# Performance work log

Hardware: AMD Instinct MI355X
Metric: run time of the kernel (lower is better)

Reference implementation:

```python
import jax, jax.numpy as jnp
import numpy as np

N_USER = 100_000
N_WALLET = 100_000
E = 1_600_000
HID, OUT = 128, 64
H, C = 4, 32  # GAT heads, per-head channels (HID // 4)
U_IN, W_IN = 16, 4
EPS = 1e-5


def _sage(x_src, x_dst, ei, w_l, b_l, w_r):
    """PyG SAGEConv (mean aggr): lin_l(mean_j x_j) + lin_r(x_i)."""
    src, dst = ei[0], ei[1]
    n = x_dst.shape[0]
    s = jax.ops.segment_sum(x_src[src], dst, num_segments=n)
    deg = jax.ops.segment_sum(jnp.ones((src.shape[0],), x_src.dtype), dst, num_segments=n)
    agg = s / jnp.maximum(deg, 1.0)[:, None]
    return agg @ w_l + b_l + x_dst @ w_r


def _bn(x, g, b):
    """BatchNorm over node dim (training-mode batch stats)."""
    m = x.mean(0)
    v = x.var(0)
    return (x - m) * jax.lax.rsqrt(v + EPS) * g + b


def _segment_softmax(logits, seg, n):
    m = jax.ops.segment_max(logits, seg, num_segments=n)
    e = jnp.exp(logits - m[seg])
    s = jax.ops.segment_sum(e, seg, num_segments=n)
    return e / (s[seg] + 1e-16)


def _gat(x, ei, w, a_src, a_dst, bias):
    """PyG GATConv with self-loops, heads concatenated. Dropout off (eval)."""
    n = x.shape[0]
    loop = jnp.arange(n, dtype=ei.dtype)
    src = jnp.concatenate([ei[0], loop])
    dst = jnp.concatenate([ei[1], loop])
    xp = (x @ w).reshape(n, H, C)                      # [n,H,C]
    al_s = (xp * a_src).sum(-1)                        # [n,H]
    al_d = (xp * a_dst).sum(-1)                        # [n,H]
    logits = jax.nn.leaky_relu(al_s[src] + al_d[dst], 0.2)  # [E+n,H]
    alpha = _segment_softmax(logits, dst, n)
    out = jax.ops.segment_sum(xp[src] * alpha[:, :, None], dst, num_segments=n)
    return out.reshape(n, H * C) + bias


def setup_inputs() -> dict:
    key = jax.random.key(0)
    ks = jax.random.split(key, 24)
    rn = lambda k, s, sc=0.05: jax.random.normal(k, s, jnp.float32) * sc
    ei = lambda k, n: jax.random.randint(k, (2, E), 0, n, jnp.int32)
    return {
        "x_user": rn(ks[0], (N_USER, U_IN), 1.0),
        "x_wallet": rn(ks[1], (N_WALLET, W_IN), 1.0),
        "w_u2w_l": rn(ks[2], (U_IN, HID)), "b_u2w": jnp.zeros((HID,), jnp.float32), "w_u2w_r": rn(ks[3], (W_IN, HID)),
        "w_w2u_l": rn(ks[4], (W_IN, HID)), "b_w2u": jnp.zeros((HID,), jnp.float32), "w_w2u_r": rn(ks[5], (U_IN, HID)),
        "w_u2u_l": rn(ks[6], (U_IN, HID)), "b_u2u": jnp.zeros((HID,), jnp.float32), "w_u2u_r": rn(ks[7], (U_IN, HID)),
        "bn_u_g": jnp.ones((HID,), jnp.float32), "bn_u_b": jnp.zeros((HID,), jnp.float32),
        "bn_w_g": jnp.ones((HID,), jnp.float32), "bn_w_b": jnp.zeros((HID,), jnp.float32),
        "gat_w": rn(ks[8], (HID, H * C)), "gat_as": rn(ks[9], (H, C)), "gat_ad": rn(ks[10], (H, C)),
        "gat_b": jnp.zeros((HID,), jnp.float32),
        "bn2_g": jnp.ones((HID,), jnp.float32), "bn2_b": jnp.zeros((HID,), jnp.float32),
        "proj_w": rn(ks[11], (HID, OUT)), "proj_b": jnp.zeros((OUT,), jnp.float32),
        "ei_uw": ei(ks[12], N_USER),   # src user -> dst wallet (both 100k)
        "ei_wu": ei(ks[13], N_WALLET),  # src wallet -> dst user
        "ei_uu": ei(ks[14], N_USER),
    }


def reference(x_user, x_wallet, w_u2w_l, b_u2w, w_u2w_r, w_w2u_l, b_w2u, w_w2u_r,
              w_u2u_l, b_u2u, w_u2u_r, bn_u_g, bn_u_b, bn_w_g, bn_w_b,
              gat_w, gat_as, gat_ad, gat_b, bn2_g, bn2_b, proj_w, proj_b,
              ei_uw, ei_wu, ei_uu):
    h_w_from_u = jax.nn.relu(_sage(x_user, x_wallet, ei_uw, w_u2w_l, b_u2w, w_u2w_r))
    h_u_from_w = jax.nn.relu(_sage(x_wallet, x_user, ei_wu, w_w2u_l, b_w2u, w_w2u_r))
    h_u_from_u = jax.nn.relu(_sage(x_user, x_user, ei_uu, w_u2u_l, b_u2u, w_u2u_r))
    h_user = _bn(h_u_from_w + h_u_from_u, bn_u_g, bn_u_b)
    _ = _bn(h_w_from_u, bn_w_g, bn_w_b)  # h_wallet: computed in torch module but unused in output
    h_user = jax.nn.relu(_gat(h_user, ei_uu, gat_w, gat_as, gat_ad, gat_b))
    h_user = _bn(h_user, bn2_g, bn2_b)
    return jax.nn.relu(h_user @ proj_w + proj_b)  # dropout = identity (eval)
```

## Files before the change

kernel.cpp:

```cpp
#include <hip/hip_runtime.h>
#include <hip/hip_bf16.h>
#include <cstdint>
#include <cstddef>

#define NN   100000
#define NE   1600000
#define CAP  48

#define NBKT 784
#define BSH  7
#define FB   8
#define BCAP 2432
#define ACHUNK 2048
#define NABLK 784

#define NTILES 1563
#define CH_BN 50
#define NSHAD 4
#define LOG2E 1.44269504088896f

typedef __attribute__((ext_vector_type(8))) short short8;
typedef __attribute__((ext_vector_type(4))) float floatx4;

__device__ inline short f2bs(float x) {
    __hip_bfloat16 h = __float2bfloat16(x);
    return *reinterpret_cast<short*>(&h);
}
__device__ inline int pack2(float a, float b) {
    return ((int)(unsigned short)f2bs(b) << 16) | (unsigned short)f2bs(a);
}
__device__ inline float bflo(unsigned p) { return __uint_as_float(p << 16); }
__device__ inline float bfhi(unsigned p) { return __uint_as_float(p & 0xFFFF0000u); }

#define OFF_PRE   ((size_t)0)
#define OFF_BKTU  ((size_t)0)
#define OFF_BKTW  ((size_t)1906688)
#define OFF_XP    ((size_t)12800000)
#define OFF_AGGU  ((size_t)12800000)
#define OFF_AGGW  ((size_t)14400000)
#define OFF_COLU  ((size_t)19200000)
#define OFF_S1    ((size_t)24000000)
#define OFF_Q1    ((size_t)24000512)
#define OFF_S2    ((size_t)24001024)
#define OFF_Q2    ((size_t)24001536)
#define OFF_CNTU  ((size_t)25600000)
#define OFF_BCUR  ((size_t)25800000)
#define OFF_ALS   ((size_t)25802112)
#define OFF_ALD   ((size_t)26202112)
#define ZBASE     OFF_BCUR
#define ZFLOATS   ((size_t)1600)
#define ZSTATS    ((size_t)2048)

__global__ void __launch_bounds__(256) bin_edges(
    const int* __restrict__ ei_u, const int* __restrict__ ei_w,
    int* __restrict__ bcur_u, int* __restrict__ bkt_u,
    int* __restrict__ bcur_w, int* __restrict__ bkt_w) {
    const int* ei = blockIdx.y ? ei_w : ei_u;
    int* bcur = blockIdx.y ? bcur_w : bcur_u;
    int* bkt  = blockIdx.y ? bkt_w  : bkt_u;
    __shared__ int lcnt[NBKT];
    __shared__ int lbuf[NBKT * FB];
    for (int i = threadIdx.x; i < NBKT; i += 256) lcnt[i] = 0;
    __syncthreads();
    int base = blockIdx.x * ACHUNK;
    #pragma unroll
    for (int k = 0; k < ACHUNK / 256; k++) {
        int e = base + k * 256 + threadIdx.x;
        if (e < NE) {
            int src = ei[e], dst = ei[NE + e];
            int b = dst >> BSH;
            int pk = ((dst & ((1 << BSH) - 1)) << 17) | src;
            int pos = atomicAdd(&lcnt[b], 1);
            if (pos < FB) lbuf[b * FB + pos] = pk;
            else {
                int g = atomicAdd(&bcur[b], 1);
                if (g < BCAP) bkt[(size_t)b * BCAP + g] = pk;
            }
        }
    }
    __syncthreads();
    int wid = threadIdx.x >> 6, lane = threadIdx.x & 63;
    const int BPW = NBKT / 4;
    int b0w = wid * BPW;
    for (int r = 0; r < BPW; r += 64) {
        int rb = r + lane;
        if (rb < BPW) {
            int b = b0w + rb;
            int c = lcnt[b];
            int nn2 = c < FB ? c : FB;
            if (nn2 > 0) {
                int g0 = atomicAdd(&bcur[b], nn2);
                for (int i2 = 0; i2 < nn2; i2++) {
                    int g = g0 + i2;
                    if (g < BCAP) bkt[(size_t)b * BCAP + g] = lbuf[b * FB + i2];
                }
            }
        }
    }
}

__global__ void __launch_bounds__(256) csr_agg(
    const int* __restrict__ bcur_u, const int* __restrict__ bkt_u,
    int* __restrict__ cnt_g, int* __restrict__ col_g,
    const float* __restrict__ xu, float* __restrict__ aggu,
    const int* __restrict__ bcur_w, const int* __restrict__ bkt_w,
    const float* __restrict__ xw, float* __restrict__ aggw) {
    int type = blockIdx.y;
    const int* bcur = type ? bcur_w : bcur_u;
    const int* bkt  = type ? bkt_w  : bkt_u;
    int B = blockIdx.x;
    int node_base = B << BSH;
    if (node_base >= NN) return;
    __shared__ int cnt[128];
    __shared__ int col[128 * CAP];
    if (threadIdx.x < 128) cnt[threadIdx.x] = 0;
    __syncthreads();
    int n = bcur[B]; if (n > BCAP) n = BCAP;
    const int* bp = bkt + (size_t)B * BCAP;
    for (int i = threadIdx.x; i < n; i += 256) {
        int p = bp[i];
        int d = p >> 17;
        int pos = atomicAdd(&cnt[d], 1);
        if (pos < CAP) col[d * CAP + pos] = p & 0x1FFFF;
    }
    __syncthreads();
    int nn_here = NN - node_base; if (nn_here > 128) nn_here = 128;
    int wv = threadIdx.x >> 6, lane = threadIdx.x & 63;

    if (type == 0) {
        if (threadIdx.x < nn_here) cnt_g[node_base + threadIdx.x] = cnt[threadIdx.x];
        int total4 = nn_here * CAP / 4;
        const int4* cs = (const int4*)col;
        int4* cg = (int4*)(col_g + (size_t)node_base * CAP);
        for (int i = threadIdx.x; i < total4; i += 256) cg[i] = cs[i];
        int j = lane >> 4, k = lane & 15;
        for (int nl = wv * 32; nl < wv * 32 + 32 && nl < nn_here; nl++) {
            int deg = cnt[nl];
            int nu = deg < CAP ? deg : CAP;
            float v0 = 0.f, v1 = 0.f, v2 = 0.f, v3 = 0.f;
            int iters = (nu + 15) >> 4;
            for (int it = 0; it < iters; it++) {
                int bb = j + (it << 4);
                int s0 = (bb < nu)      ? col[nl * CAP + bb]      : 0;
                int s1 = (bb + 4 < nu)  ? col[nl * CAP + bb + 4]  : 0;
                int s2 = (bb + 8 < nu)  ? col[nl * CAP + bb + 8]  : 0;
                int s3 = (bb + 12 < nu) ? col[nl * CAP + bb + 12] : 0;
                float x0 = xu[(size_t)s0 * 16 + k];
                float x1 = xu[(size_t)s1 * 16 + k];
                float x2 = xu[(size_t)s2 * 16 + k];
                float x3 = xu[(size_t)s3 * 16 + k];
                if (bb < nu)      v0 += x0;
                if (bb + 4 < nu)  v1 += x1;
                if (bb + 8 < nu)  v2 += x2;
                if (bb + 12 < nu) v3 += x3;
            }
            float v = (v0 + v1) + (v2 + v3);
            v += __shfl_xor(v, 16, 64);
            v += __shfl_xor(v, 32, 64);
            if (lane < 16)
                aggu[(size_t)(node_base + nl) * 16 + lane] = v / fmaxf((float)deg, 1.f);
        }
    } else {
        int j = lane >> 2, k = lane & 3;
        for (int nl = wv * 32; nl < wv * 32 + 32 && nl < nn_here; nl++) {
            int deg = cnt[nl];
            int nw = deg < CAP ? deg : CAP;
            float v = 0.f;
            int iters = (nw + 15) >> 4;
            for (int it = 0; it < iters; it++) {
                int bb = j + (it << 4);
                int s = (bb < nw) ? col[nl * CAP + bb] : 0;
                float x = xw[(size_t)s * 4 + k];
                if (bb < nw) v += x;
            }
            v += __shfl_xor(v, 4, 64);
            v += __shfl_xor(v, 8, 64);
            v += __shfl_xor(v, 16, 64);
            v += __shfl_xor(v, 32, 64);
            if (lane < 4)
                aggw[(size_t)(node_base + nl) * 4 + lane] = v / fmaxf((float)deg, 1.f);
        }
    }
}

__global__ void __launch_bounds__(256, 2) sage_gemm(
    const float* __restrict__ aggu, const float* __restrict__ aggw,
    const float* __restrict__ xu,
    const float* __restrict__ wl_w2u, const float* __restrict__ b_w2u, const float* __restrict__ wr_w2u,
    const float* __restrict__ wl_u2u, const float* __restrict__ b_u2u, const float* __restrict__ wr_u2u,
    __hip_bfloat16* __restrict__ pre) {
    __shared__ short lw[16 * 64 * 8];
    __shared__ short la[64 * 136];
    int tid = threadIdx.x;
    for (int idx = tid; idx < 8192; idx += 256) {
        int mat = idx >> 12;
        int k = (idx >> 7) & 31, n = idx & 127;
        float w;
        if (mat == 0)
            w = (k < 4) ? wl_w2u[k * 128 + n] : (k < 20 ? wr_w2u[(k - 4) * 128 + n] : 0.f);
        else
            w = (k < 16) ? wl_u2u[k * 128 + n] : wr_u2u[(k - 16) * 128 + n];
        int t = n >> 4, l15 = n & 15, q = (k >> 3) & 3, j = k & 7;
        lw[((mat * 8 + t) * 64 + q * 16 + l15) * 8 + j] = f2bs(w);
    }
    __syncthreads();
    int wv = tid >> 6, lane = tid & 63;
    int quad = lane >> 4, l15 = lane & 15;
    short8 w1[8], w2[8];
    #pragma unroll
    for (int t = 0; t < 8; t++) {
        w1[t] = *(const short8*)&lw[(t * 64 + lane) * 8];
        w2[t] = *(const short8*)&lw[((8 + t) * 64 + lane) * 8];
    }
    float bw[8], bu[8];
    #pragma unroll
    for (int t = 0; t < 8; t++) {
        bw[t] = b_w2u[t * 16 + l15];
        bu[t] = b_u2u[t * 16 + l15];
    }
    for (int tile = blockIdx.x; tile < NTILES; tile += gridDim.x) {
        int nbase = tile * 64;
        __syncthreads();
        {
            int node = tid >> 2, p = tid & 3;
            int gn = nbase + node;
            float4 v = make_float4(0.f, 0.f, 0.f, 0.f);
            if (gn < NN) v = *(const float4*)&xu[(size_t)gn * 16 + 4 * p];
            int2 pk; pk.x = pack2(v.x, v.y); pk.y = pack2(v.z, v.w);
            *(int2*)&la[node * 136 + 4 + 4 * p] = pk;
            *(int2*)&la[node * 136 + 48 + 4 * p] = pk;
        }
        {
            int node = tid >> 2, p = tid & 3;
            int gn = nbase + node;
            float4 v = make_float4(0.f, 0.f, 0.f, 0.f);
            if (gn < NN) v = *(const float4*)&aggu[(size_t)gn * 16 + 4 * p];
            int2 pk; pk.x = pack2(v.x, v.y); pk.y = pack2(v.z, v.w);
            *(int2*)&la[node * 136 + 32 + 4 * p] = pk;
        }
        if (tid < 64) {
            int node = tid, gn = nbase + node;
            float4 v = make_float4(0.f, 0.f, 0.f, 0.f);
            if (gn < NN) v = *(const float4*)&aggw[(size_t)gn * 4];
            int2 pk; pk.x = pack2(v.x, v.y); pk.y = pack2(v.z, v.w);
            *(int2*)&la[node * 136 + 0] = pk;
            int2 z; z.x = 0; z.y = 0;
            *(int2*)&la[node * 136 + 20] = z;
            *(int2*)&la[node * 136 + 24] = z;
            *(int2*)&la[node * 136 + 28] = z;
        }
        __syncthreads();
        short8 af1 = *(const short8*)&la[(wv * 16 + l15) * 136 + quad * 8];
        short8 af2 = *(const short8*)&la[(wv * 16 + l15) * 136 + 32 + quad * 8];
        floatx4 acc1[8], acc2[8];
        #pragma unroll
        for (int t = 0; t < 8; t++) {
            acc1[t] = (floatx4){0.f, 0.f, 0.f, 0.f};
            acc2[t] = (floatx4){0.f, 0.f, 0.f, 0.f};
        }
        #pragma unroll
        for (int t = 0; t < 8; t++) {
            acc1[t] = __builtin_amdgcn_mfma_f32_16x16x32_bf16(af1, w1[t], acc1[t], 0, 0, 0);
            acc2[t] = __builtin_amdgcn_mfma_f32_16x16x32_bf16(af2, w2[t], acc2[t], 0, 0, 0);
        }
        __syncthreads();
        #pragma unroll
        for (int t = 0; t < 8; t++)
            #pragma unroll
            for (int r = 0; r < 4; r++) {
                float v1 = fmaxf(acc1[t][r] + bw[t], 0.f);
                float v2 = fmaxf(acc2[t][r] + bu[t], 0.f);
                la[(wv * 16 + quad * 4 + r) * 136 + t * 16 + l15] = f2bs(v1 + v2);
            }
        __syncthreads();
        #pragma unroll
        for (int c = 0; c < 4; c++) {
            int idx = c * 256 + tid;
            int node = idx >> 4, f8 = (idx & 15) * 8;
            int gn = nbase + node;
            if (gn < NN)
                *(int4*)(pre + (size_t)gn * 128 + f8) = *(const int4*)&la[node * 136 + f8];
        }
    }
}

__global__ void __launch_bounds__(256) bn_stats_pre2(const unsigned* __restrict__ x2,
                                                     float* __restrict__ sum, float* __restrict__ sq) {
    int f2 = threadIdx.x & 63, half = threadIdx.x >> 6;
    int n0 = blockIdx.x * CH_BN;
    float s0 = 0.f, q0 = 0.f, s1 = 0.f, q1 = 0.f;
    for (int i = n0 + half; i < n0 + CH_BN; i += 4) {
        unsigned p = x2[(size_t)i * 64 + f2];
        float v0 = bflo(p), v1 = bfhi(p);
        s0 += v0; q0 += v0 * v0; s1 += v1; q1 += v1 * v1;
    }
    __shared__ float a0[256], c0[256], a1[256], c1[256];
    a0[threadIdx.x] = s0; c0[threadIdx.x] = q0;
    a1[threadIdx.x] = s1; c1[threadIdx.x] = q1;
    __syncthreads();
    if (half == 0) {
        for (int h = 1; h < 4; h++) {
            s0 += a0[h * 64 + f2]; q0 += c0[h * 64 + f2];
            s1 += a1[h * 64 + f2]; q1 += c1[h * 64 + f2];
        }
        int sh = (blockIdx.x & (NSHAD - 1)) << 7;
        atomicAdd(&sum[sh + 2 * f2], s0);     atomicAdd(&sq[sh + 2 * f2], q0);
        atomicAdd(&sum[sh + 2 * f2 + 1], s1); atomicAdd(&sq[sh + 2 * f2 + 1], q1);
    }
}

__global__ void __launch_bounds__(256) bn_stats_act2(const unsigned* __restrict__ x2,
                                                     const float* __restrict__ gb,
                                                     float* __restrict__ sum, float* __restrict__ sq) {
    int f2 = threadIdx.x & 63, half = threadIdx.x >> 6;
    int n0 = blockIdx.x * CH_BN;
    float gb0 = gb[2 * f2], gb1 = gb[2 * f2 + 1];
    float s0 = 0.f, q0 = 0.f, s1 = 0.f, q1 = 0.f;
    for (int i = n0 + half; i < n0 + CH_BN; i += 4) {
        unsigned p = x2[(size_t)i * 64 + f2];
        float v0 = fmaxf(bflo(p) + gb0, 0.f), v1 = fmaxf(bfhi(p) + gb1, 0.f);
        s0 += v0; q0 += v0 * v0; s1 += v1; q1 += v1 * v1;
    }
    __shared__ float a0[256], c0[256], a1[256], c1[256];
    a0[threadIdx.x] = s0; c0[threadIdx.x] = q0;
    a1[threadIdx.x] = s1; c1[threadIdx.x] = q1;
    __syncthreads();
    if (half == 0) {
        for (int h = 1; h < 4; h++) {
            s0 += a0[h * 64 + f2]; q0 += c0[h * 64 + f2];
            s1 += a1[h * 64 + f2]; q1 += c1[h * 64 + f2];
        }
        int sh = (blockIdx.x & (NSHAD - 1)) << 7;
        atomicAdd(&sum[sh + 2 * f2], s0);     atomicAdd(&sq[sh + 2 * f2], q0);
        atomicAdd(&sum[sh + 2 * f2 + 1], s1); atomicAdd(&sq[sh + 2 * f2 + 1], q1);
    }
}

__global__ void __launch_bounds__(256, 2) gemm_al(
    const unsigned* __restrict__ pre2, const float* __restrict__ s1, const float* __restrict__ q1,
    const float* __restrict__ bng, const float* __restrict__ bnb,
    const float* __restrict__ gw, const float* __restrict__ gas, const float* __restrict__ gad,
    __hip_bfloat16* __restrict__ xp, float* __restrict__ al_s, float* __restrict__ al_d) {
    __shared__ short lw[32 * 64 * 8];
    __shared__ short la[64 * 136];
    __shared__ float lsc[128], lsh[128];
    int tid = threadIdx.x;
    if (tid < 128) {
        float sv = s1[tid] + s1[128 + tid] + s1[256 + tid] + s1[384 + tid];
        float qv = q1[tid] + q1[128 + tid] + q1[256 + tid] + q1[384 + tid];
        float m = sv * (1.0f / NN);
        float v = qv * (1.0f / NN) - m * m;
        float sc = bng[tid] * rsqrtf(v + 1e-5f);
        lsc[tid] = sc; lsh[tid] = bnb[tid] - m * sc;
    }
    for (int idx = tid; idx < 16384; idx += 256) {
        int k = idx >> 7, n = idx & 127;
        int t = n >> 4, l15 = n & 15, s = k >> 5, q = (k >> 3) & 3, j = k & 7;
        lw[(((t * 4 + s) * 64) + q * 16 + l15) * 8 + j] = f2bs(gw[idx]);
    }
    __syncthreads();
    int wv = tid >> 6, lane = tid & 63;
    int quad = lane >> 4, l15 = lane & 15;
    short8 wfrag[8][4];
    #pragma unroll
    for (int t = 0; t < 8; t++)
        #pragma unroll
        for (int s = 0; s < 4; s++)
            wfrag[t][s] = *(const short8*)&lw[((t * 4 + s) * 64 + lane) * 8];
    float asv[8], adv[8];
    #pragma unroll
    for (int t = 0; t < 8; t++) {
        asv[t] = gas[t * 16 + l15] * LOG2E;
        adv[t] = gad[t * 16 + l15] * LOG2E;
    }
    for (int tile = blockIdx.x; tile < NTILES; tile += gridDim.x) {
        int nbase = tile * 64;
        __syncthreads();
        #pragma unroll
        for (int c = 0; c < 8; c++) {
            int idx = c * 256 + tid;
            int node = idx >> 5, g = idx & 31;
            uint2 pp = make_uint2(0u, 0u);
            int gn = nbase + node;
            if (gn < NN) pp = *(const uint2*)&pre2[(size_t)gn * 64 + 2 * g];
            int f = 4 * g;
            float v0 = bflo(pp.x), v1 = bfhi(pp.x), v2 = bflo(pp.y), v3 = bfhi(pp.y);
            int2 pk;
            pk.x = pack2(v0 * lsc[f] + lsh[f],         v1 * lsc[f + 1] + lsh[f + 1]);
            pk.y = pack2(v2 * lsc[f + 2] + lsh[f + 2], v3 * lsc[f + 3] + lsh[f + 3]);
            *(int2*)&la[node * 136 + f] = pk;
        }
        __syncthreads();
        short8 af[4];
        #pragma unroll
        for (int s = 0; s < 4; s++)
            af[s] = *(const short8*)&la[(wv * 16 + l15) * 136 + s * 32 + quad * 8];
        floatx4 acc[8];
        #pragma unroll
        for (int t = 0; t < 8; t++) acc[t] = (floatx4){0.f, 0.f, 0.f, 0.f};
        #pragma unroll
        for (int s = 0; s < 4; s++)
            #pragma unroll
            for (int t = 0; t < 8; t++)
                acc[t] = __builtin_amdgcn_mfma_f32_16x16x32_bf16(af[s], wfrag[t][s], acc[t], 0, 0, 0);
        #pragma unroll
        for (int r = 0; r < 4; r++) {
            int node = nbase + wv * 16 + quad * 4 + r;
            #pragma unroll
            for (int h = 0; h < 4; h++) {
                float vs = acc[2 * h][r] * asv[2 * h] + acc[2 * h + 1][r] * asv[2 * h + 1];
                float vd = acc[2 * h][r] * adv[2 * h] + acc[2 * h + 1][r] * adv[2 * h + 1];
                #pragma unroll
                for (int m = 8; m >= 1; m >>= 1) {
                    vs += __shfl_xor(vs, m, 64);
                    vd += __shfl_xor(vd, m, 64);
                }
                if (l15 == 0 && node < NN) {
                    al_s[(size_t)node * 4 + h] = vs;
                    al_d[(size_t)node * 4 + h] = vd;
                }
            }
        }
        __syncthreads();
        #pragma unroll
        for (int t = 0; t < 8; t++)
            #pragma unroll
            for (int r = 0; r < 4; r++)
                la[(wv * 16 + quad * 4 + r) * 136 + t * 16 + l15] = f2bs(acc[t][r]);
        __syncthreads();
        #pragma unroll
        for (int c = 0; c < 4; c++) {
            int idx = c * 256 + tid;
            int node = idx >> 4, f8 = (idx & 15) * 8;
            int gn = nbase + node;
            if (gn < NN)
                *(int4*)(xp + (size_t)gn * 128 + f8) = *(const int4*)&la[node * 136 + f8];
        }
    }
}

__global__ void __launch_bounds__(256, 2) gemm_proj(
    const unsigned* __restrict__ gat2, const float* __restrict__ gb,
    const float* __restrict__ s2, const float* __restrict__ q2,
    const float* __restrict__ bng, const float* __restrict__ bnb,
    const float* __restrict__ pw, const float* __restrict__ pb,
    float* __restrict__ out) {
    __shared__ short lw[16 * 64 * 8];
    __shared__ short la[64 * 136];
    __shared__ float lsc[128], lsh[128], lgb[128];
    int tid = threadIdx.x;
    if (tid < 128) {
        float sv = s2[tid] + s2[128 + tid] + s2[256 + tid] + s2[384 + tid];
        float qv = q2[tid] + q2[128 + tid] + q2[256 + tid] + q2[384 + tid];
        float m = sv * (1.0f / NN);
        float v = qv * (1.0f / NN) - m * m;
        float sc = bng[tid] * rsqrtf(v + 1e-5f);
        lsc[tid] = sc; lsh[tid] = bnb[tid] - m * sc;
        lgb[tid] = gb[tid];
    }
    for (int idx = tid; idx < 8192; idx += 256) {
        int k = idx >> 6, n = idx & 63;
        int t = n >> 4, l15 = n & 15, s = k >> 5, q = (k >> 3) & 3, j = k & 7;
        lw[(((t * 4 + s) * 64) + q * 16 + l15) * 8 + j] = f2bs(pw[idx]);
    }
    __syncthreads();
    int wv = tid >> 6, lane = tid & 63;
    int quad = lane >> 4, l15 = lane & 15;
    short8 wfrag[4][4];
    #pragma unroll
    for (int t = 0; t < 4; t++)
        #pragma unroll
        for (int s = 0; s < 4; s++)
            wfrag[t][s] = *(const short8*)&lw[((t * 4 + s) * 64 + lane) * 8];
    float pbv[4];
    #pragma unroll
    for (int t = 0; t < 4; t++) pbv[t] = pb[t * 16 + l15];
    for (int tile = blockIdx.x; tile < NTILES; tile += gridDim.x) {
        int nbase = tile * 64;
        __syncthreads();
        #pragma unroll
        for (int c = 0; c < 8; c++) {
            int idx = c * 256 + tid;
            int node = idx >> 5, g = idx & 31;
            uint2 pp = make_uint2(0u, 0u);
            int gn = nbase + node;
            if (gn < NN) pp = *(const uint2*)&gat2[(size_t)gn * 64 + 2 * g];
            int f = 4 * g;
            float h0 = fmaxf(bflo(pp.x) + lgb[f],     0.f) * lsc[f]     + lsh[f];
            float h1 = fmaxf(bfhi(pp.x) + lgb[f + 1], 0.f) * lsc[f + 1] + lsh[f + 1];
            float h2 = fmaxf(bflo(pp.y) + lgb[f + 2], 0.f) * lsc[f + 2] + lsh[f + 2];
            float h3 = fmaxf(bfhi(pp.y) + lgb[f + 3], 0.f) * lsc[f + 3] + lsh[f + 3];
            int2 pk; pk.x = pack2(h0, h1); pk.y = pack2(h2, h3);
            *(int2*)&la[node * 136 + f] = pk;
        }
        __syncthreads();
        short8 af[4];
        #pragma unroll
        for (int s = 0; s < 4; s++)
            af[s] = *(const short8*)&la[(wv * 16 + l15) * 136 + s * 32 + quad * 8];
        floatx4 acc[4];
        #pragma unroll
        for (int t = 0; t < 4; t++) acc[t] = (floatx4){0.f, 0.f, 0.f, 0.f};
        #pragma unroll
        for (int s = 0; s < 4; s++)
            #pragma unroll
            for (int t = 0; t < 4; t++)
                acc[t] = __builtin_amdgcn_mfma_f32_16x16x32_bf16(af[s], wfrag[t][s], acc[t], 0, 0, 0);
        #pragma unroll
        for (int r = 0; r < 4; r++) {
            int gn = nbase + wv * 16 + quad * 4 + r;
            if (gn < NN) {
                #pragma unroll
                for (int t = 0; t < 4; t++)
                    out[(size_t)gn * 64 + t * 16 + l15] = fmaxf(acc[t][r] + pbv[t], 0.f);
            }
        }
    }
}

__global__ void __launch_bounds__(256) gat_gather(
    const int* __restrict__ cnt_u, const int* __restrict__ col_u,
    const float* __restrict__ al_s, const float* __restrict__ al_d,
    const unsigned* __restrict__ xp2, unsigned* __restrict__ gout2) {
    int i = (blockIdx.x * 256 + threadIdx.x) >> 6;
    int lane = threadIdx.x & 63;
    int g = lane >> 4, q = lane & 15;
    int h = q >> 2;
    float ad = al_d[(size_t)i * 4 + h];
    int deg = cnt_u[i];
    int n = deg < CAP ? deg : CAP;
    int mycol = (lane < n) ? col_u[(size_t)i * CAP + lane] : 0;
    float a0 = 0.f, a1 = 0.f, a2 = 0.f, a3 = 0.f;
    float a4 = 0.f, a5 = 0.f, a6 = 0.f, a7 = 0.f, den = 0.f;
    if (g == 0) {
        float l = al_s[(size_t)i * 4 + h] + ad;
        float e = exp2f(fmaxf(l, 0.2f * l));
        uint4 p = *(const uint4*)&xp2[(size_t)i * 64 + 4 * q];
        a0 = e * bflo(p.x); a1 = e * bfhi(p.x);
        a2 = e * bflo(p.y); a3 = e * bfhi(p.y);
        a4 = e * bflo(p.z); a5 = e * bfhi(p.z);
        a6 = e * bflo(p.w); a7 = e * bfhi(p.w);
        den = e;
    }
    for (int b = 0; b < n; b += 16) {
        int s[4]; float A[4]; uint4 p[4];
        #pragma unroll
        for (int u = 0; u < 4; u++)
            s[u] = __shfl(mycol, b + 4 * u + g, 64);
        #pragma unroll
        for (int u = 0; u < 4; u++)
            A[u] = al_s[(size_t)s[u] * 4 + h];
        #pragma unroll
        for (int u = 0; u < 4; u++)
            p[u] = *(const uint4*)&xp2[(size_t)s[u] * 64 + 4 * q];
        #pragma unroll
        for (int u = 0; u < 4; u++) {
            float l = A[u] + ad;
            float e = (b + 4 * u + g < n) ? exp2f(fmaxf(l, 0.2f * l)) : 0.f;
            a0 += e * bflo(p[u].x); a1 += e * bfhi(p[u].x);
            a2 += e * bflo(p[u].y); a3 += e * bfhi(p[u].y);
            a4 += e * bflo(p[u].z); a5 += e * bfhi(p[u].z);
            a6 += e * bflo(p[u].w); a7 += e * bfhi(p[u].w);
            den += e;
        }
    }
    a0 += __shfl_xor(a0, 16, 64); a0 += __shfl_xor(a0, 32, 64);
    a1 += __shfl_xor(a1, 16, 64); a1 += __shfl_xor(a1, 32, 64);
    a2 += __shfl_xor(a2, 16, 64); a2 += __shfl_xor(a2, 32, 64);
    a3 += __shfl_xor(a3, 16, 64); a3 += __shfl_xor(a3, 32, 64);
    a4 += __shfl_xor(a4, 16, 64); a4 += __shfl_xor(a4, 32, 64);
    a5 += __shfl_xor(a5, 16, 64); a5 += __shfl_xor(a5, 32, 64);
    a6 += __shfl_xor(a6, 16, 64); a6 += __shfl_xor(a6, 32, 64);
    a7 += __shfl_xor(a7, 16, 64); a7 += __shfl_xor(a7, 32, 64);
    den += __shfl_xor(den, 16, 64); den += __shfl_xor(den, 32, 64);
    if (g == 0) {
        float r = 1.0f / (den + 1e-16f);
        uint4 o;
        o.x = (unsigned)pack2(a0 * r, a1 * r);
        o.y = (unsigned)pack2(a2 * r, a3 * r);
        o.z = (unsigned)pack2(a4 * r, a5 * r);
        o.w = (unsigned)pack2(a6 * r, a7 * r);
        *(uint4*)&gout2[(size_t)i * 64 + 4 * q] = o;
    }
}

extern "C" void kernel_launch(void* const* d_in, const int* in_sizes, int n_in,
                              void* d_out, int out_size, void* d_ws, size_t ws_size,
                              hipStream_t stream) {
    const float* x_user   = (const float*)d_in[0];
    const float* x_wallet = (const float*)d_in[1];
    const float* w_w2u_l  = (const float*)d_in[5];
    const float* b_w2u    = (const float*)d_in[6];
    const float* w_w2u_r  = (const float*)d_in[7];
    const float* w_u2u_l  = (const float*)d_in[8];
    const float* b_u2u    = (const float*)d_in[9];
    const float* w_u2u_r  = (const float*)d_in[10];
    const float* bn_u_g   = (const float*)d_in[11];
    const float* bn_u_b   = (const float*)d_in[12];
    const float* gat_w    = (const float*)d_in[15];
    const float* gat_as   = (const float*)d_in[16];
    const float* gat_ad   = (const float*)d_in[17];
    const float* gat_b    = (const float*)d_in[18];
    const float* bn2_g    = (const float*)d_in[19];
    const float* bn2_b    = (const float*)d_in[20];
    const float* proj_w   = (const float*)d_in[21];
    const float* proj_b   = (const float*)d_in[22];
    const int* ei_wu      = (const int*)d_in[24];
    const int* ei_uu      = (const int*)d_in[25];
    float* out = (float*)d_out;
    float* ws  = (float*)d_ws;

    unsigned* pre2 = (unsigned*)(ws + OFF_PRE);
    __hip_bfloat16* pre = (__hip_bfloat16*)(ws + OFF_PRE);
    int*   bkt_u  = (int*)(ws + OFF_BKTU);
    int*   bkt_w  = (int*)(ws + OFF_BKTW);
    __hip_bfloat16* xp = (__hip_bfloat16*)(ws + OFF_XP);
    unsigned* xp2 = (unsigned*)(ws + OFF_XP);
    float* aggu = ws + OFF_AGGU;
    float* aggw = ws + OFF_AGGW;
    int*   col_u  = (int*)(ws + OFF_COLU);
    int*   cnt_u  = (int*)(ws + OFF_CNTU);
    int*   bcur_u = (int*)(ws + OFF_BCUR);
    int*   bcur_w = (int*)(ws + OFF_BCUR) + 800;
    float* al_s = ws + OFF_ALS, *al_d = ws + OFF_ALD;
    float* s1 = ws + OFF_S1, *q1 = ws + OFF_Q1;
    float* s2 = ws + OFF_S2, *q2 = ws + OFF_Q2;

    hipMemsetAsync(ws + ZBASE, 0, ZFLOATS * sizeof(float), stream);
    hipMemsetAsync(ws + OFF_S1, 0, ZSTATS * sizeof(float), stream);

    bin_edges<<<dim3(NABLK, 2), 256, 0, stream>>>(ei_uu, ei_wu, bcur_u, bkt_u, bcur_w, bkt_w);

    csr_agg<<<dim3(NBKT, 2), 256, 0, stream>>>(
        bcur_u, bkt_u, cnt_u, col_u, x_user, aggu,
        bcur_w, bkt_w, x_wallet, aggw);

    sage_gemm<<<512, 256, 0, stream>>>(
        aggu, aggw, x_user, w_w2u_l, b_w2u, w_w2u_r, w_u2u_l, b_u2u, w_u2u_r, pre);

    bn_stats_pre2<<<NN / CH_BN, 256, 0, stream>>>(pre2, s1, q1);

    gemm_al<<<512, 256, 0, stream>>>(pre2, s1, q1, bn_u_g, bn_u_b,
                                     gat_w, gat_as, gat_ad, xp, al_s, al_d);

    unsigned* gat2 = pre2;
    gat_gather<<<NN / 4, 256, 0, stream>>>(cnt_u, col_u, al_s, al_d, xp2, gat2);

    bn_stats_act2<<<NN / CH_BN, 256, 0, stream>>>(gat2, gat_b, s2, q2);

    gemm_proj<<<512, 256, 0, stream>>>(gat2, gat_b, s2, q2, bn2_g, bn2_b,
                                       proj_w, proj_b, out);
}
```

Baseline: 466.1 us.

## Fuse BN statistics into SAGE GEMM epilogue and enlarge edge-binning chunks

Computes the per-feature sum and sum-of-squares for the first batch norm inside the sage_gemm epilogue. Values are accumulated in registers, reduced through shared-memory atomics, then added to the sharded global buffers. This removes the separate bn_stats_pre2 kernel and its full re-read of the pre-activation tensor. Separately, the edge-binning kernel now uses larger chunks with half as many blocks, and FB is raised. The fused path adds register pressure and atomics to a kernel limited to two blocks per CU.

```diff
diff --git a/kernel.cpp b/kernel.cpp
--- a/kernel.cpp
+++ b/kernel.cpp
@@ -9,10 +9,10 @@
 
 #define NBKT 784
 #define BSH  7
-#define FB   8
+#define FB   12
 #define BCAP 2432
-#define ACHUNK 2048
-#define NABLK 784
+#define ACHUNK 4096
+#define NABLK 391
 
 #define NTILES 1563
 #define CH_BN 50
@@ -188,9 +188,11 @@
     const float* __restrict__ xu,
     const float* __restrict__ wl_w2u, const float* __restrict__ b_w2u, const float* __restrict__ wr_w2u,
     const float* __restrict__ wl_u2u, const float* __restrict__ b_u2u, const float* __restrict__ wr_u2u,
-    __hip_bfloat16* __restrict__ pre) {
+    __hip_bfloat16* __restrict__ pre,
+    float* __restrict__ bnsum, float* __restrict__ bnsq) {
     __shared__ short lw[16 * 64 * 8];
     __shared__ short la[64 * 136];
+    __shared__ float lbs[128], lbq[128];
     int tid = threadIdx.x;
     for (int idx = tid; idx < 8192; idx += 256) {
         int mat = idx >> 12;
@@ -203,6 +205,7 @@
         int t = n >> 4, l15 = n & 15, q = (k >> 3) & 3, j = k & 7;
         lw[((mat * 8 + t) * 64 + q * 16 + l15) * 8 + j] = f2bs(w);
     }
+    if (tid < 128) { lbs[tid] = 0.f; lbq[tid] = 0.f; }
     __syncthreads();
     int wv = tid >> 6, lane = tid & 63;
     int quad = lane >> 4, l15 = lane & 15;
@@ -218,6 +221,9 @@
         bw[t] = b_w2u[t * 16 + l15];
         bu[t] = b_u2u[t * 16 + l15];
     }
+    float sE[8], qE[8];
+    #pragma unroll
+    for (int t = 0; t < 8; t++) { sE[t] = 0.f; qE[t] = 0.f; }
     for (int tile = blockIdx.x; tile < NTILES; tile += gridDim.x) {
         int nbase = tile * 64;
         __syncthreads();
@@ -270,7 +276,13 @@
             for (int r = 0; r < 4; r++) {
                 float v1 = fmaxf(acc1[t][r] + bw[t], 0.f);
                 float v2 = fmaxf(acc2[t][r] + bu[t], 0.f);
-                la[(wv * 16 + quad * 4 + r) * 136 + t * 16 + l15] = f2bs(v1 + v2);
+                short vv = f2bs(v1 + v2);
+                la[(wv * 16 + quad * 4 + r) * 136 + t * 16 + l15] = vv;
+                int node = nbase + wv * 16 + quad * 4 + r;
+                if (node < NN) {
+                    float vr = __uint_as_float(((unsigned)(unsigned short)vv) << 16);
+                    sE[t] += vr; qE[t] += vr * vr;
+                }
             }
         __syncthreads();
         #pragma unroll
@@ -282,30 +294,17 @@
                 *(int4*)(pre + (size_t)gn * 128 + f8) = *(const int4*)&la[node * 136 + f8];
         }
     }
-}
-
-__global__ void __launch_bounds__(256) bn_stats_pre2(const unsigned* __restrict__ x2,
-                                                     float* __restrict__ sum, float* __restrict__ sq) {
-    int f2 = threadIdx.x & 63, half = threadIdx.x >> 6;
-    int n0 = blockIdx.x * CH_BN;
-    float s0 = 0.f, q0 = 0.f, s1 = 0.f, q1 = 0.f;
-    for (int i = n0 + half; i < n0 + CH_BN; i += 4) {
-        unsigned p = x2[(size_t)i * 64 + f2];
-        float v0 = bflo(p), v1 = bfhi(p);
-        s0 += v0; q0 += v0 * v0; s1 += v1; q1 += v1 * v1;
-    }
-    __shared__ float a0[256], c0[256], a1[256], c1[256];
-    a0[threadIdx.x] = s0; c0[threadIdx.x] = q0;
-    a1[threadIdx.x] = s1; c1[threadIdx.x] = q1;
-    __syncthreads();
-    if (half == 0) {
-        for (int h = 1; h < 4; h++) {
-            s0 += a0[h * 64 + f2]; q0 += c0[h * 64 + f2];
-            s1 += a1[h * 64 + f2]; q1 += c1[h * 64 + f2];
-        }
+    __syncthreads();
+    #pragma unroll
+    for (int t = 0; t < 8; t++) {
+        atomicAdd(&lbs[t * 16 + l15], sE[t]);
+        atomicAdd(&lbq[t * 16 + l15], qE[t]);
+    }
+    __syncthreads();
+    if (tid < 128) {
         int sh = (blockIdx.x & (NSHAD - 1)) << 7;
-        atomicAdd(&sum[sh + 2 * f2], s0);     atomicAdd(&sq[sh + 2 * f2], q0);
-        atomicAdd(&sum[sh + 2 * f2 + 1], s1); atomicAdd(&sq[sh + 2 * f2 + 1], q1);
+        atomicAdd(&bnsum[sh + tid], lbs[tid]);
+        atomicAdd(&bnsq[sh + tid], lbq[tid]);
     }
 }
 
@@ -636,9 +635,8 @@
         bcur_w, bkt_w, x_wallet, aggw);
 
     sage_gemm<<<512, 256, 0, stream>>>(
-        aggu, aggw, x_user, w_w2u_l, b_w2u, w_w2u_r, w_u2u_l, b_u2u, w_u2u_r, pre);
-
-    bn_stats_pre2<<<NN / CH_BN, 256, 0, stream>>>(pre2, s1, q1);
+        aggu, aggw, x_user, w_w2u_l, b_w2u, w_w2u_r, w_u2u_l, b_u2u, w_u2u_r,
+        pre, s1, q1);
 
     gemm_al<<<512, 256, 0, stream>>>(pre2, s1, q1, bn_u_g, bn_u_b,
                                      gat_w, gat_as, gat_ad, xp, al_s, al_d);
```

Result: faster. 427.9 us (-8.2%).
